# Performance work log

Measured on AMD Instinct MI355X. Metric: run time of the kernel, lower is better.

## Reference

```python
import jax, jax.numpy as jnp
import numpy as np

N_ATOMS = 100000
N_BONDS = 200000
MAX_NB = 6
N_ATOM_FEATS = 39
N_BOND_FEATS = 11
HIDDEN = 128
DEPTH = 6


def setup_inputs() -> dict:
    key = jax.random.key(0)
    k = jax.random.split(key, 8)
    fatoms = jax.random.normal(k[0], (N_ATOMS, N_ATOM_FEATS), dtype=jnp.float32)
    fbonds = jax.random.normal(k[1], (N_BONDS, N_ATOM_FEATS + N_BOND_FEATS), dtype=jnp.float32)
    agraph = jax.random.randint(k[2], (N_ATOMS, MAX_NB), 0, N_BONDS, dtype=jnp.int32)
    bgraph = jax.random.randint(k[3], (N_BONDS, MAX_NB), 0, N_BONDS, dtype=jnp.int32)
    s_i = 1.0 / np.sqrt(N_ATOM_FEATS + N_BOND_FEATS)
    s_h = 1.0 / np.sqrt(HIDDEN)
    s_o = 1.0 / np.sqrt(N_ATOM_FEATS + HIDDEN)
    W_i = jax.random.uniform(k[4], (HIDDEN, N_ATOM_FEATS + N_BOND_FEATS), jnp.float32, -s_i, s_i)
    W_h = jax.random.uniform(k[5], (HIDDEN, HIDDEN), jnp.float32, -s_h, s_h)
    W_o = jax.random.uniform(k[6], (HIDDEN, N_ATOM_FEATS + HIDDEN), jnp.float32, -s_o, s_o)
    b_o = jax.random.uniform(k[7], (HIDDEN,), jnp.float32, -s_o, s_o)
    return {"fatoms": fatoms, "fbonds": fbonds, "agraph": agraph, "bgraph": bgraph,
            "W_i": W_i, "W_h": W_h, "W_o": W_o, "b_o": b_o}


def reference(fatoms, fbonds, agraph, bgraph, W_i, W_h, W_o, b_o):
    # Input message per directed bond: [n_bonds, hidden]
    binput = fbonds @ W_i.T
    message = jax.nn.relu(binput)
    # Message passing: gather neighbor bond messages, sum, linear, residual-add input, ReLU
    for _ in range(DEPTH - 1):
        nei = jnp.take(message, bgraph, axis=0).sum(axis=1)   # [n_bonds, hidden]
        message = jax.nn.relu(binput + nei @ W_h.T)
    # Aggregate incoming bond messages per atom
    a_nei = jnp.take(message, agraph, axis=0).sum(axis=1)      # [n_atoms, hidden]
    atom_input = jnp.concatenate([fatoms, a_nei], axis=1)      # dropout is identity at eval
    atom_h = jax.nn.relu(atom_input @ W_o.T + b_o)
    return atom_h
```

## Files before the change

kernel.cpp:

```cpp
#include <hip/hip_runtime.h>

#define N_ATOMS   100000
#define N_BONDS   200000
#define MAX_NB    6
#define AF        39
#define BFEAT     50
#define H         128
#define DEPTH     6
#define KS_I      2
#define KS_IH     6
#define KS_O      6
#define FBW       64

typedef unsigned short ushort_t;
typedef unsigned int   uint_t;

typedef __attribute__((ext_vector_type(8))) short  bf16x8;
typedef __attribute__((ext_vector_type(4))) float  f32x4;

__device__ inline uint_t cvt_pk(float lo, float hi) {
    uint_t r;
    asm("v_cvt_pk_bf16_f32 %0, %1, %2" : "=v"(r) : "v"(lo), "v"(hi));
    return r;
}
__device__ inline ushort_t f2bf(float f) { return (ushort_t)cvt_pk(f, f); }

__device__ inline void addv(float* a, uint4 v) {
    union { uint_t u; float f; } c;
    c.u = v.x << 16;          a[0] += c.f;
    c.u = v.x & 0xffff0000u;  a[1] += c.f;
    c.u = v.y << 16;          a[2] += c.f;
    c.u = v.y & 0xffff0000u;  a[3] += c.f;
    c.u = v.z << 16;          a[4] += c.f;
    c.u = v.z & 0xffff0000u;  a[5] += c.f;
    c.u = v.w << 16;          a[6] += c.f;
    c.u = v.w & 0xffff0000u;  a[7] += c.f;
}

__global__ __launch_bounds__(256) void k_pack(const float* __restrict__ W_i,
                                              const float* __restrict__ W_h,
                                              const float* __restrict__ W_o,
                                              ushort_t* __restrict__ pWi,
                                              ushort_t* __restrict__ pWih,
                                              ushort_t* __restrict__ pWo) {
    int id = blockIdx.x * 256 + threadIdx.x;
    int mat;
    ushort_t* dst;
    if (id < 1024)      { mat = 0; dst = pWi; }
    else if (id < 4096) { mat = 1; dst = pWih; id -= 1024; }
    else                { mat = 2; dst = pWo;  id -= 4096; }
    const int lane = id & 63;
    const int nt   = (id >> 6) & 7;
    const int ks   = id >> 9;
    const int n  = nt * 16 + (lane & 15);
    const int k0 = ks * 32 + (lane >> 4) * 8;
    float v[8];
#pragma unroll
    for (int j = 0; j < 8; ++j) {
        const int k = k0 + j;
        float x = 0.f;
        if (mat == 0) {
            if (k < BFEAT) x = W_i[n * BFEAT + k];
        } else if (mat == 1) {
            if (k < BFEAT)     x = W_i[n * BFEAT + k];
            else if (k >= FBW) x = W_h[n * H + (k - FBW)];
        } else {
            if (k < H)           x = W_o[(size_t)n * (AF + H) + AF + k];
            else if (k < H + AF) x = W_o[(size_t)n * (AF + H) + (k - H)];
        }
        v[j] = x;
    }
    uint4 u;
    u.x = cvt_pk(v[0], v[1]); u.y = cvt_pk(v[2], v[3]);
    u.z = cvt_pk(v[4], v[5]); u.w = cvt_pk(v[6], v[7]);
    ((uint4*)dst)[id] = u;
}

__global__ __launch_bounds__(256) void k_binput(const float* __restrict__ fbonds,
                                                const ushort_t* __restrict__ pWi,
                                                ushort_t* __restrict__ fbb,
                                                ushort_t* __restrict__ msg0) {
    __shared__ __align__(16) ushort_t sAC[64][136];
    const int t = threadIdx.x;
    const int b0 = blockIdx.x * 64;

    for (int i = t; i < 64 * 25; i += 256) {
        const int row = i / 25, j = i % 25;
        const float2 v = *(const float2*)(fbonds + (size_t)(b0 + row) * BFEAT + j * 2);
        *(uint_t*)&sAC[row][j * 2] = cvt_pk(v.x, v.y);
    }
    for (int i = t; i < 64 * 7; i += 256) {
        const int row = i / 7, c = BFEAT + (i % 7) * 2;
        *(uint_t*)&sAC[row][c] = 0u;
    }
    __syncthreads();

    for (int i = t; i < 64 * 8; i += 256) {
        const int row = i >> 3, c0 = (i & 7) * 8;
        *(uint4*)(fbb + (size_t)(b0 + row) * FBW + c0) = *(const uint4*)&sAC[row][c0];
    }

    const int w    = t >> 6;
    const int lane = t & 63;
    const int col  = lane & 15;
    const int kg   = lane >> 4;
    const int m    = 16 * w + col;

    f32x4 acc[8];
#pragma unroll
    for (int nt = 0; nt < 8; ++nt) acc[nt] = (f32x4){0.f, 0.f, 0.f, 0.f};
    bf16x8 af[KS_I];
#pragma unroll
    for (int ks = 0; ks < KS_I; ++ks)
        af[ks] = *(const bf16x8*)&sAC[m][ks * 32 + kg * 8];
#pragma unroll
    for (int ks = 0; ks < KS_I; ++ks) {
#pragma unroll
        for (int nt = 0; nt < 8; ++nt) {
            const bf16x8 b = *(const bf16x8*)(pWi + (((size_t)(ks * 8 + nt) * 64 + lane) * 8));
            acc[nt] = __builtin_amdgcn_mfma_f32_16x16x32_bf16(af[ks], b, acc[nt], 0, 0, 0);
        }
    }
    __syncthreads();

    const int row0 = kg * 4;
#pragma unroll
    for (int nt = 0; nt < 8; ++nt)
#pragma unroll
        for (int r = 0; r < 4; ++r)
            sAC[16 * w + row0 + r][nt * 16 + col] = f2bf(fmaxf(acc[nt][r], 0.f));
    __syncthreads();

    for (int i = t; i < 64 * 16; i += 256) {
        const int row = i >> 4, c0 = (i & 15) * 8;
        *(uint4*)(msg0 + (size_t)(b0 + row) * H + c0) = *(const uint4*)&sAC[row][c0];
    }
}

__global__ __launch_bounds__(256) void k_mp(const ushort_t* __restrict__ msg_in,
                                            const int* __restrict__ bgraph,
                                            const ushort_t* __restrict__ pWih,
                                            const ushort_t* __restrict__ fbb,
                                            ushort_t* __restrict__ msg_out) {
    __shared__ __align__(16) ushort_t sAC[64][200];
    __shared__ int sIdx[64][MAX_NB];
    const int t = threadIdx.x;
    const int b0 = blockIdx.x * 64;

    for (int i = t; i < 64 * 8; i += 256) {
        const int row = i >> 3, c0 = (i & 7) * 8;
        *(uint4*)&sAC[row][c0] = *(const uint4*)(fbb + (size_t)(b0 + row) * FBW + c0);
    }
    for (int i = t; i < 64 * MAX_NB; i += 256)
        sIdx[i / MAX_NB][i % MAX_NB] = bgraph[(size_t)b0 * MAX_NB + i];
    __syncthreads();

    {
        const int bi = t >> 4;
        const int c0 = (t & 15) * 8;
#pragma unroll
        for (int p = 0; p < 4; p += 2) {
            const int iA = p * 16 + bi;
            const int iB = iA + 16;
            uint4 vA[MAX_NB], vB[MAX_NB];
#pragma unroll
            for (int j = 0; j < MAX_NB; ++j)
                vA[j] = *(const uint4*)(msg_in + (size_t)sIdx[iA][j] * H + c0);
#pragma unroll
            for (int j = 0; j < MAX_NB; ++j)
                vB[j] = *(const uint4*)(msg_in + (size_t)sIdx[iB][j] * H + c0);
            float a[8], b[8];
#pragma unroll
            for (int q = 0; q < 8; ++q) { a[q] = 0.f; b[q] = 0.f; }
#pragma unroll
            for (int j = 0; j < MAX_NB; ++j) addv(a, vA[j]);
#pragma unroll
            for (int j = 0; j < MAX_NB; ++j) addv(b, vB[j]);
            uint4 ua, ub;
            ua.x = cvt_pk(a[0], a[1]); ua.y = cvt_pk(a[2], a[3]);
            ua.z = cvt_pk(a[4], a[5]); ua.w = cvt_pk(a[6], a[7]);
            ub.x = cvt_pk(b[0], b[1]); ub.y = cvt_pk(b[2], b[3]);
            ub.z = cvt_pk(b[4], b[5]); ub.w = cvt_pk(b[6], b[7]);
            *(uint4*)&sAC[iA][FBW + c0] = ua;
            *(uint4*)&sAC[iB][FBW + c0] = ub;
        }
    }
    __syncthreads();

    const int w    = t >> 6;
    const int lane = t & 63;
    const int col  = lane & 15;
    const int kg   = lane >> 4;
    const int m    = 16 * w + col;

    f32x4 acc[8];
#pragma unroll
    for (int nt = 0; nt < 8; ++nt) acc[nt] = (f32x4){0.f, 0.f, 0.f, 0.f};
    bf16x8 af[KS_IH];
#pragma unroll
    for (int ks = 0; ks < KS_IH; ++ks)
        af[ks] = *(const bf16x8*)&sAC[m][ks * 32 + kg * 8];
#pragma unroll
    for (int ks = 0; ks < KS_IH; ++ks) {
#pragma unroll
        for (int nt = 0; nt < 8; ++nt) {
            const bf16x8 b = *(const bf16x8*)(pWih + (((size_t)(ks * 8 + nt) * 64 + lane) * 8));
            acc[nt] = __builtin_amdgcn_mfma_f32_16x16x32_bf16(af[ks], b, acc[nt], 0, 0, 0);
        }
    }
    const int row0 = kg * 4;
#pragma unroll
    for (int nt = 0; nt < 8; ++nt)
#pragma unroll
        for (int r = 0; r < 4; ++r)
            sAC[16 * w + row0 + r][nt * 16 + col] = f2bf(fmaxf(acc[nt][r], 0.f));
    __syncthreads();

    for (int i = t; i < 64 * 16; i += 256) {
        const int row = i >> 4, c0 = (i & 15) * 8;
        *(uint4*)(msg_out + (size_t)(b0 + row) * H + c0) = *(const uint4*)&sAC[row][c0];
    }
}

__global__ __launch_bounds__(256) void k_out(const ushort_t* __restrict__ msg,
                                             const int* __restrict__ agraph,
                                             const float* __restrict__ fatoms,
                                             const ushort_t* __restrict__ pWo,
                                             const float* __restrict__ b_o,
                                             float* __restrict__ out) {
    __shared__ __align__(16) unsigned char smem[64 * 132 * 4];
    ushort_t (*sA)[200] = (ushort_t(*)[200])smem;
    float    (*sC)[132] = (float(*)[132])smem;
    __shared__ int sIdx[64][MAX_NB];
    const int t = threadIdx.x;
    const int a0 = blockIdx.x * 64;

    for (int i = t; i < 64 * MAX_NB; i += 256) {
        const int a = a0 + i / MAX_NB;
        sIdx[i / MAX_NB][i % MAX_NB] = (a < N_ATOMS) ? agraph[(size_t)a * MAX_NB + (i % MAX_NB)] : 0;
    }
    for (int i = t; i < 64 * 64; i += 256) {
        const int row = i >> 6, c = i & 63;
        const int a = a0 + row;
        float x = 0.f;
        if (c < AF && a < N_ATOMS) x = fatoms[(size_t)a * AF + c];
        sA[row][H + c] = f2bf(x);
    }
    __syncthreads();

    {
        const int bi = t >> 4;
        const int c0 = (t & 15) * 8;
#pragma unroll
        for (int p = 0; p < 4; p += 2) {
            const int iA = p * 16 + bi;
            const int iB = iA + 16;
            uint4 vA[MAX_NB], vB[MAX_NB];
#pragma unroll
            for (int j = 0; j < MAX_NB; ++j)
                vA[j] = *(const uint4*)(msg + (size_t)sIdx[iA][j] * H + c0);
#pragma unroll
            for (int j = 0; j < MAX_NB; ++j)
                vB[j] = *(const uint4*)(msg + (size_t)sIdx[iB][j] * H + c0);
            float a[8], b[8];
#pragma unroll
            for (int q = 0; q < 8; ++q) { a[q] = 0.f; b[q] = 0.f; }
#pragma unroll
            for (int j = 0; j < MAX_NB; ++j) addv(a, vA[j]);
#pragma unroll
            for (int j = 0; j < MAX_NB; ++j) addv(b, vB[j]);
            uint4 ua, ub;
            ua.x = cvt_pk(a[0], a[1]); ua.y = cvt_pk(a[2], a[3]);
            ua.z = cvt_pk(a[4], a[5]); ua.w = cvt_pk(a[6], a[7]);
            ub.x = cvt_pk(b[0], b[1]); ub.y = cvt_pk(b[2], b[3]);
            ub.z = cvt_pk(b[4], b[5]); ub.w = cvt_pk(b[6], b[7]);
            *(uint4*)&sA[iA][c0] = ua;
            *(uint4*)&sA[iB][c0] = ub;
        }
    }
    __syncthreads();

    const int w    = t >> 6;
    const int lane = t & 63;
    const int col  = lane & 15;
    const int kg   = lane >> 4;
    const int m    = 16 * w + col;

    f32x4 acc[8];
#pragma unroll
    for (int nt = 0; nt < 8; ++nt) acc[nt] = (f32x4){0.f, 0.f, 0.f, 0.f};
#pragma unroll
    for (int ks = 0; ks < KS_O; ++ks) {
        const bf16x8 a = *(const bf16x8*)&sA[m][ks * 32 + kg * 8];
#pragma unroll
        for (int nt = 0; nt < 8; ++nt) {
            const bf16x8 b = *(const bf16x8*)(pWo + (((size_t)(ks * 8 + nt) * 64 + lane) * 8));
            acc[nt] = __builtin_amdgcn_mfma_f32_16x16x32_bf16(a, b, acc[nt], 0, 0, 0);
        }
    }
    __syncthreads();

    const int row0 = kg * 4;
#pragma unroll
    for (int nt = 0; nt < 8; ++nt)
#pragma unroll
        for (int r = 0; r < 4; ++r)
            sC[16 * w + row0 + r][nt * 16 + col] = acc[nt][r];
    __syncthreads();

    const float4* bo4 = (const float4*)b_o;
    for (int i = t; i < 64 * 16; i += 256) {
        const int row = i >> 4, c0 = (i & 15) * 8;
        const int a = a0 + row;
        if (a < N_ATOMS) {
            const float* cp = &sC[row][c0];
            const float4 b1 = bo4[c0 >> 2];
            const float4 b2 = bo4[(c0 >> 2) + 1];
            float4 o1, o2;
            o1.x = cp[0] + b1.x; o1.y = cp[1] + b1.y; o1.z = cp[2] + b1.z; o1.w = cp[3] + b1.w;
            o2.x = cp[4] + b2.x; o2.y = cp[5] + b2.y; o2.z = cp[6] + b2.z; o2.w = cp[7] + b2.w;
            o1.x = o1.x > 0.f ? o1.x : 0.f; o1.y = o1.y > 0.f ? o1.y : 0.f;
            o1.z = o1.z > 0.f ? o1.z : 0.f; o1.w = o1.w > 0.f ? o1.w : 0.f;
            o2.x = o2.x > 0.f ? o2.x : 0.f; o2.y = o2.y > 0.f ? o2.y : 0.f;
            o2.z = o2.z > 0.f ? o2.z : 0.f; o2.w = o2.w > 0.f ? o2.w : 0.f;
            float* op = out + (size_t)a * H + c0;
            *(float4*)op = o1;
            *(float4*)(op + 4) = o2;
        }
    }
}

extern "C" void kernel_launch(void* const* d_in, const int* in_sizes, int n_in,
                              void* d_out, int out_size, void* d_ws, size_t ws_size,
                              hipStream_t stream) {
    const float* fatoms = (const float*)d_in[0];
    const float* fbonds = (const float*)d_in[1];
    const int*   agraph = (const int*)d_in[2];
    const int*   bgraph = (const int*)d_in[3];
    const float* W_i    = (const float*)d_in[4];
    const float* W_h    = (const float*)d_in[5];
    const float* W_o    = (const float*)d_in[6];
    const float* b_o    = (const float*)d_in[7];
    float* out = (float*)d_out;

    const size_t MSG_BYTES = (size_t)N_BONDS * H * sizeof(ushort_t);
    const size_t FBB_BYTES = (size_t)N_BONDS * FBW * sizeof(ushort_t);
    char* ws = (char*)d_ws;
    ushort_t* m0   = (ushort_t*)(ws);
    ushort_t* m1   = (ushort_t*)(ws + MSG_BYTES);
    ushort_t* fbb  = (ushort_t*)(ws + 2 * MSG_BYTES);
    ushort_t* pWi  = (ushort_t*)(ws + 2 * MSG_BYTES + FBB_BYTES);
    ushort_t* pWih = (ushort_t*)(ws + 2 * MSG_BYTES + FBB_BYTES + 16 * 1024);
    ushort_t* pWo  = (ushort_t*)(ws + 2 * MSG_BYTES + FBB_BYTES + 64 * 1024);

    k_pack<<<28, 256, 0, stream>>>(W_i, W_h, W_o, pWi, pWih, pWo);
    k_binput<<<N_BONDS / 64, 256, 0, stream>>>(fbonds, pWi, fbb, m0);

    ushort_t* cur = m0;
    ushort_t* nxt = m1;
    for (int d = 0; d < DEPTH - 1; ++d) {
        k_mp<<<N_BONDS / 64, 256, 0, stream>>>(cur, bgraph, pWih, fbb, nxt);
        ushort_t* tmp = cur; cur = nxt; nxt = tmp;
    }

    k_out<<<(N_ATOMS + 63) / 64, 256, 0, stream>>>(cur, agraph, fatoms, pWo, b_o, out);
}
```

Before: 475.9 us.

## Load bond/atom feature fragments directly from global and shrink LDS for occupancy

```diff
diff --git a/kernel.cpp b/kernel.cpp
--- a/kernel.cpp
+++ b/kernel.cpp
@@ -11,6 +11,7 @@
 #define KS_IH     6
 #define KS_O      6
 #define FBW       64
+#define FAW       64
 
 typedef unsigned short ushort_t;
 typedef unsigned int   uint_t;
@@ -76,6 +77,29 @@
     ((uint4*)dst)[id] = u;
 }
 
+__global__ __launch_bounds__(256) void k_fab(const float* __restrict__ fatoms,
+                                             ushort_t* __restrict__ fab) {
+    const int t = threadIdx.x;
+    const int a0 = blockIdx.x * 64;
+    const int row = t >> 2;
+    const int c0 = (t & 3) * 16;
+    const int a = a0 + row;
+    if (a >= N_ATOMS) return;
+    float v[16];
+#pragma unroll
+    for (int j = 0; j < 16; ++j) {
+        const int c = c0 + j;
+        v[j] = (c < AF) ? fatoms[(size_t)a * AF + c] : 0.f;
+    }
+    uint4 u0, u1;
+    u0.x = cvt_pk(v[0],  v[1]);  u0.y = cvt_pk(v[2],  v[3]);
+    u0.z = cvt_pk(v[4],  v[5]);  u0.w = cvt_pk(v[6],  v[7]);
+    u1.x = cvt_pk(v[8],  v[9]);  u1.y = cvt_pk(v[10], v[11]);
+    u1.z = cvt_pk(v[12], v[13]); u1.w = cvt_pk(v[14], v[15]);
+    *(uint4*)(fab + (size_t)a * FAW + c0)     = u0;
+    *(uint4*)(fab + (size_t)a * FAW + c0 + 8) = u1;
+}
+
 __global__ __launch_bounds__(256) void k_binput(const float* __restrict__ fbonds,
                                                 const ushort_t* __restrict__ pWi,
                                                 ushort_t* __restrict__ fbb,
@@ -137,20 +161,16 @@
     }
 }
 
-__global__ __launch_bounds__(256) void k_mp(const ushort_t* __restrict__ msg_in,
-                                            const int* __restrict__ bgraph,
-                                            const ushort_t* __restrict__ pWih,
-                                            const ushort_t* __restrict__ fbb,
-                                            ushort_t* __restrict__ msg_out) {
-    __shared__ __align__(16) ushort_t sAC[64][200];
+__global__ __launch_bounds__(256, 8) void k_mp(const ushort_t* __restrict__ msg_in,
+                                               const int* __restrict__ bgraph,
+                                               const ushort_t* __restrict__ pWih,
+                                               const ushort_t* __restrict__ fbb,
+                                               ushort_t* __restrict__ msg_out) {
+    __shared__ __align__(16) ushort_t sAC[64][136];
     __shared__ int sIdx[64][MAX_NB];
     const int t = threadIdx.x;
     const int b0 = blockIdx.x * 64;
 
-    for (int i = t; i < 64 * 8; i += 256) {
-        const int row = i >> 3, c0 = (i & 7) * 8;
-        *(uint4*)&sAC[row][c0] = *(const uint4*)(fbb + (size_t)(b0 + row) * FBW + c0);
-    }
     for (int i = t; i < 64 * MAX_NB; i += 256)
         sIdx[i / MAX_NB][i % MAX_NB] = bgraph[(size_t)b0 * MAX_NB + i];
     __syncthreads();
@@ -181,11 +201,10 @@
             ua.z = cvt_pk(a[4], a[5]); ua.w = cvt_pk(a[6], a[7]);
             ub.x = cvt_pk(b[0], b[1]); ub.y = cvt_pk(b[2], b[3]);
             ub.z = cvt_pk(b[4], b[5]); ub.w = cvt_pk(b[6], b[7]);
-            *(uint4*)&sAC[iA][FBW + c0] = ua;
-            *(uint4*)&sAC[iB][FBW + c0] = ub;
-        }
-    }
-    __syncthreads();
+            *(uint4*)&sAC[iA][c0] = ua;
+            *(uint4*)&sAC[iB][c0] = ub;
+        }
+    }
 
     const int w    = t >> 6;
     const int lane = t & 63;
@@ -193,13 +212,17 @@
     const int kg   = lane >> 4;
     const int m    = 16 * w + col;
 
+    bf16x8 af[KS_IH];
+    af[0] = *(const bf16x8*)(fbb + (size_t)(b0 + m) * FBW + kg * 8);
+    af[1] = *(const bf16x8*)(fbb + (size_t)(b0 + m) * FBW + 32 + kg * 8);
+    __syncthreads();
+#pragma unroll
+    for (int ks = 2; ks < KS_IH; ++ks)
+        af[ks] = *(const bf16x8*)&sAC[m][(ks - 2) * 32 + kg * 8];
+
     f32x4 acc[8];
 #pragma unroll
     for (int nt = 0; nt < 8; ++nt) acc[nt] = (f32x4){0.f, 0.f, 0.f, 0.f};
-    bf16x8 af[KS_IH];
-#pragma unroll
-    for (int ks = 0; ks < KS_IH; ++ks)
-        af[ks] = *(const bf16x8*)&sAC[m][ks * 32 + kg * 8];
 #pragma unroll
     for (int ks = 0; ks < KS_IH; ++ks) {
 #pragma unroll
@@ -222,15 +245,13 @@
     }
 }
 
-__global__ __launch_bounds__(256) void k_out(const ushort_t* __restrict__ msg,
-                                             const int* __restrict__ agraph,
-                                             const float* __restrict__ fatoms,
-                                             const ushort_t* __restrict__ pWo,
-                                             const float* __restrict__ b_o,
-                                             float* __restrict__ out) {
-    __shared__ __align__(16) unsigned char smem[64 * 132 * 4];
-    ushort_t (*sA)[200] = (ushort_t(*)[200])smem;
-    float    (*sC)[132] = (float(*)[132])smem;
+__global__ __launch_bounds__(256, 8) void k_out(const ushort_t* __restrict__ msg,
+                                                const int* __restrict__ agraph,
+                                                const ushort_t* __restrict__ fab,
+                                                const ushort_t* __restrict__ pWo,
+                                                const float* __restrict__ b_o,
+                                                float* __restrict__ out) {
+    __shared__ __align__(16) ushort_t sA[64][136];
     __shared__ int sIdx[64][MAX_NB];
     const int t = threadIdx.x;
     const int a0 = blockIdx.x * 64;
@@ -238,13 +259,6 @@
     for (int i = t; i < 64 * MAX_NB; i += 256) {
         const int a = a0 + i / MAX_NB;
         sIdx[i / MAX_NB][i % MAX_NB] = (a < N_ATOMS) ? agraph[(size_t)a * MAX_NB + (i % MAX_NB)] : 0;
-    }
-    for (int i = t; i < 64 * 64; i += 256) {
-        const int row = i >> 6, c = i & 63;
-        const int a = a0 + row;
-        float x = 0.f;
-        if (c < AF && a < N_ATOMS) x = fatoms[(size_t)a * AF + c];
-        sA[row][H + c] = f2bf(x);
     }
     __syncthreads();
 
@@ -278,54 +292,46 @@
             *(uint4*)&sA[iB][c0] = ub;
         }
     }
-    __syncthreads();
 
     const int w    = t >> 6;
     const int lane = t & 63;
     const int col  = lane & 15;
     const int kg   = lane >> 4;
     const int m    = 16 * w + col;
+    const int am   = a0 + m;
+    const size_t amc = (size_t)((am < N_ATOMS) ? am : 0);
+
+    bf16x8 af[KS_O];
+    af[4] = *(const bf16x8*)(fab + amc * FAW + kg * 8);
+    af[5] = *(const bf16x8*)(fab + amc * FAW + 32 + kg * 8);
+    __syncthreads();
+#pragma unroll
+    for (int ks = 0; ks < 4; ++ks)
+        af[ks] = *(const bf16x8*)&sA[m][ks * 32 + kg * 8];
 
     f32x4 acc[8];
 #pragma unroll
     for (int nt = 0; nt < 8; ++nt) acc[nt] = (f32x4){0.f, 0.f, 0.f, 0.f};
 #pragma unroll
     for (int ks = 0; ks < KS_O; ++ks) {
-        const bf16x8 a = *(const bf16x8*)&sA[m][ks * 32 + kg * 8];
 #pragma unroll
         for (int nt = 0; nt < 8; ++nt) {
             const bf16x8 b = *(const bf16x8*)(pWo + (((size_t)(ks * 8 + nt) * 64 + lane) * 8));
-            acc[nt] = __builtin_amdgcn_mfma_f32_16x16x32_bf16(a, b, acc[nt], 0, 0, 0);
-        }
-    }
-    __syncthreads();
-
-    const int row0 = kg * 4;
-#pragma unroll
-    for (int nt = 0; nt < 8; ++nt)
-#pragma unroll
-        for (int r = 0; r < 4; ++r)
-            sC[16 * w + row0 + r][nt * 16 + col] = acc[nt][r];
-    __syncthreads();
-
-    const float4* bo4 = (const float4*)b_o;
-    for (int i = t; i < 64 * 16; i += 256) {
-        const int row = i >> 4, c0 = (i & 15) * 8;
-        const int a = a0 + row;
-        if (a < N_ATOMS) {
-            const float* cp = &sC[row][c0];
-            const float4 b1 = bo4[c0 >> 2];
-            const float4 b2 = bo4[(c0 >> 2) + 1];
-            float4 o1, o2;
-            o1.x = cp[0] + b1.x; o1.y = cp[1] + b1.y; o1.z = cp[2] + b1.z; o1.w = cp[3] + b1.w;
-            o2.x = cp[4] + b2.x; o2.y = cp[5] + b2.y; o2.z = cp[6] + b2.z; o2.w = cp[7] + b2.w;
-            o1.x = o1.x > 0.f ? o1.x : 0.f; o1.y = o1.y > 0.f ? o1.y : 0.f;
-            o1.z = o1.z > 0.f ? o1.z : 0.f; o1.w = o1.w > 0.f ? o1.w : 0.f;
-            o2.x = o2.x > 0.f ? o2.x : 0.f; o2.y = o2.y > 0.f ? o2.y : 0.f;
-            o2.z = o2.z > 0.f ? o2.z : 0.f; o2.w = o2.w > 0.f ? o2.w : 0.f;
-            float* op = out + (size_t)a * H + c0;
-            *(float4*)op = o1;
-            *(float4*)(op + 4) = o2;
+            acc[nt] = __builtin_amdgcn_mfma_f32_16x16x32_bf16(af[ks], b, acc[nt], 0, 0, 0);
+        }
+    }
+
+    float bias[8];
+#pragma unroll
+    for (int nt = 0; nt < 8; ++nt) bias[nt] = b_o[nt * 16 + col];
+    const int rowbase = a0 + 16 * w + kg * 4;
+#pragma unroll
+    for (int nt = 0; nt < 8; ++nt) {
+#pragma unroll
+        for (int r = 0; r < 4; ++r) {
+            const int arow = rowbase + r;
+            if (arow < N_ATOMS)
+                out[(size_t)arow * H + nt * 16 + col] = fmaxf(acc[nt][r] + bias[nt], 0.f);
         }
     }
 }
@@ -345,15 +351,19 @@
 
     const size_t MSG_BYTES = (size_t)N_BONDS * H * sizeof(ushort_t);
     const size_t FBB_BYTES = (size_t)N_BONDS * FBW * sizeof(ushort_t);
+    const size_t FAB_BYTES = (size_t)N_ATOMS * FAW * sizeof(ushort_t);
     char* ws = (char*)d_ws;
     ushort_t* m0   = (ushort_t*)(ws);
     ushort_t* m1   = (ushort_t*)(ws + MSG_BYTES);
     ushort_t* fbb  = (ushort_t*)(ws + 2 * MSG_BYTES);
-    ushort_t* pWi  = (ushort_t*)(ws + 2 * MSG_BYTES + FBB_BYTES);
-    ushort_t* pWih = (ushort_t*)(ws + 2 * MSG_BYTES + FBB_BYTES + 16 * 1024);
-    ushort_t* pWo  = (ushort_t*)(ws + 2 * MSG_BYTES + FBB_BYTES + 64 * 1024);
+    ushort_t* fab  = (ushort_t*)(ws + 2 * MSG_BYTES + FBB_BYTES);
+    char*     wb   = ws + 2 * MSG_BYTES + FBB_BYTES + FAB_BYTES;
+    ushort_t* pWi  = (ushort_t*)(wb);
+    ushort_t* pWih = (ushort_t*)(wb + 16 * 1024);
+    ushort_t* pWo  = (ushort_t*)(wb + 64 * 1024);
 
     k_pack<<<28, 256, 0, stream>>>(W_i, W_h, W_o, pWi, pWih, pWo);
+    k_fab<<<(N_ATOMS + 63) / 64, 256, 0, stream>>>(fatoms, fab);
     k_binput<<<N_BONDS / 64, 256, 0, stream>>>(fbonds, pWi, fbb, m0);
 
     ushort_t* cur = m0;
@@ -363,5 +373,5 @@
         ushort_t* tmp = cur; cur = nxt; nxt = tmp;
     }
 
-    k_out<<<(N_ATOMS + 63) / 64, 256, 0, stream>>>(cur, agraph, fatoms, pWo, b_o, out);
-}
+    k_out<<<(N_ATOMS + 63) / 64, 256, 0, stream>>>(cur, agraph, fab, pWo, b_o, out);
+}
```

Result: slower. 710.8 us (+49.4%).
